# Performance work log

Measured on AMD Instinct MI355X. Metric: run time of the kernel, lower is better.

The kernel has to match this reference:

```python
import jax, jax.numpy as jnp
import numpy as np

N_TOKENS = 16384
D_MODEL = 2048
N_EXPERTS = 64
TOP_K = 8
TAU = 1.0
HYSTERESIS = 0.1
LAMBDA_TAX = 0.04
ALPHA_DAMPING = 0.7
SINKHORN_ITERS = 10


def setup_inputs() -> dict:
    key = jax.random.key(0)
    kx, kw, kb, kp, km = jax.random.split(key, 5)
    x = jax.random.normal(kx, (N_TOKENS, D_MODEL), dtype=jnp.float32)
    # LazyLinear(n_experts): weight [E, D], bias [E]
    W = jax.random.normal(kw, (N_EXPERTS, D_MODEL), dtype=jnp.float32) * (1.0 / np.sqrt(D_MODEL))
    b = jax.random.normal(kb, (N_EXPERTS,), dtype=jnp.float32) * 0.01
    # prev_probs buffer: a valid probability distribution per token
    prev_probs = jax.nn.softmax(jax.random.normal(kp, (N_TOKENS, N_EXPERTS), dtype=jnp.float32), axis=-1)
    # prev_mask buffer: exactly k experts active per token (what forward produces)
    scores = jax.random.normal(km, (N_TOKENS, N_EXPERTS), dtype=jnp.float32)
    idx = jax.lax.top_k(scores, TOP_K)[1]
    prev_mask = jnp.zeros((N_TOKENS, N_EXPERTS), dtype=bool).at[jnp.arange(N_TOKENS)[:, None], idx].set(True)
    return {"x": x, "W": W, "b": b, "prev_probs": prev_probs, "prev_mask": prev_mask}


def _router_probs(x, W, b, prev_probs, prev_mask):
    n = x.shape[0]
    logits = x @ W.T + b                               # [N, E]
    logits = logits - jnp.mean(logits, axis=-1, keepdims=True)
    M = jax.nn.softmax(logits / TAU, axis=-1)
    # Exact analytical gradient correction (correlation tax)
    C = M.T @ M                                        # [E, E]
    C = C * (1.0 - jnp.eye(N_EXPERTS, dtype=C.dtype))  # fill_diagonal_(0)
    grad_m = 4.0 * (M @ C)
    exact_grad = M * grad_m - M * jnp.sum(M * grad_m, axis=-1, keepdims=True)
    logits = logits - LAMBDA_TAX * exact_grad
    M = jax.nn.softmax(logits / TAU, axis=-1)
    # Convergent Sinkhorn-Knopp (10 fixed iterations)
    def body(i, M):
        M = M / jnp.clip(jnp.sum(M, axis=0, keepdims=True), 1e-12)
        M = M * (N_EXPERTS / n)
        M = M / jnp.clip(jnp.sum(M, axis=1, keepdims=True), 1e-12)
        return M
    M = jax.lax.fori_loop(0, SINKHORN_ITERS, body, M)
    # Momental damping with previous probs
    M = (1.0 - ALPHA_DAMPING) * prev_probs + ALPHA_DAMPING * M
    # Hysteresis blend with previous mask
    prev = prev_mask.astype(M.dtype)
    denom = jnp.clip(jnp.sum(prev, axis=-1, keepdims=True), 1.0)
    M = (1.0 - HYSTERESIS) * M + HYSTERESIS * (prev / denom)
    M = M / jnp.clip(jnp.sum(M, axis=-1, keepdims=True), 1e-12)
    return M


def reference(x, W, b, prev_probs, prev_mask):
    M = _router_probs(x, W, b, prev_probs, prev_mask)
    idx = jax.lax.top_k(M, TOP_K)[1]                   # [N, k]
    n = M.shape[0]
    mask = jnp.zeros(M.shape, dtype=bool).at[jnp.arange(n)[:, None], idx].set(True)
    return M, mask
```

## Files before the change

### kernel.cpp

```cpp
#include <hip/hip_runtime.h>
#include <math.h>

#define NT 16384
#define DM 2048
#define NE 64
#define TOPK 8
#define LTAX 0.04f
#define HYST 0.1f
#define ALPHA 0.7f

typedef unsigned int u32;
typedef unsigned short u16;
typedef unsigned long long u64;
typedef __attribute__((ext_vector_type(8))) short bf16x8;
typedef __attribute__((ext_vector_type(4))) float f32x4;

__device__ __forceinline__ float warp4_sum(float v) {
  v += __shfl_xor(v, 1); v += __shfl_xor(v, 2); return v;
}
__device__ __forceinline__ float warp4_max(float v) {
  v = fmaxf(v, __shfl_xor(v, 1)); v = fmaxf(v, __shfl_xor(v, 2)); return v;
}
__device__ __forceinline__ u16 f2bf(float f) {
  u32 u = __float_as_uint(f);
  return (u16)((u + 0x7fffu + ((u >> 16) & 1u)) >> 16);
}
__device__ __forceinline__ float bf2f(u16 h) { return __uint_as_float(((u32)h) << 16); }

__device__ __forceinline__ void split3(float a, short& h, short& m, short& l) {
  u16 hh = f2bf(a);  float r1 = a - bf2f(hh);
  u16 mm = f2bf(r1); float r2 = r1 - bf2f(mm);
  h = (short)hh; m = (short)mm; l = (short)f2bf(r2);
}

__device__ __forceinline__ u64 to_fx(float v) {
  return (u64)__double2ll_rn((double)v * 4294967296.0);
}

__global__ void k_init(const float* __restrict__ W, u16* __restrict__ Wh,
                       u16* __restrict__ Wm, u16* __restrict__ Wl,
                       u64* __restrict__ zp) {
  const int bid = blockIdx.x, tid = threadIdx.x;
  if (bid < 128) {
    int idx = (bid * 256 + tid) * 4;
    float4 v = *(const float4*)(W + idx);
    short h[4], m[4], l[4];
    split3(v.x, h[0], m[0], l[0]);
    split3(v.y, h[1], m[1], l[1]);
    split3(v.z, h[2], m[2], l[2]);
    split3(v.w, h[3], m[3], l[3]);
    *(ushort4*)(Wh + idx) = make_ushort4((u16)h[0], (u16)h[1], (u16)h[2], (u16)h[3]);
    *(ushort4*)(Wm + idx) = make_ushort4((u16)m[0], (u16)m[1], (u16)m[2], (u16)m[3]);
    *(ushort4*)(Wl + idx) = make_ushort4((u16)l[0], (u16)l[1], (u16)l[2], (u16)l[3]);
  } else {
    int i = (bid - 128) * 256 + tid;
    if (i < 26624) zp[i] = 0ull;
  }
}

__launch_bounds__(256, 5)
__global__ void k_gemm(const float* __restrict__ x, const u16* __restrict__ Whg,
                       const u16* __restrict__ Wmg, const u16* __restrict__ Wlg,
                       float* __restrict__ Lpart) {
  __shared__ __align__(16) u16 XS[15360];
  const int tid = threadIdx.x;
  const int bid = blockIdx.x;
  const int tile = bid >> 3, ks = bid & 7;
  const int row0 = tile * 64;
  const int k0 = ks * 256;
  const int lane = tid & 63, w = tid >> 6, l15 = lane & 15, l4 = lane >> 4;
  const int srow = tid >> 2, c8 = (tid & 3) * 8;
  const int stoff = srow * 40 + c8;

  f32x4 accA[4], accB[4];
#pragma unroll
  for (int eb = 0; eb < 4; eb++) { accA[eb] = (f32x4)0.f; accB[eb] = (f32x4)0.f; }

  float4 xq0, xq1;
  uint4 whv, wmv, wlv;
  const float* xrowp = x + (size_t)(row0 + srow) * DM + k0 + c8;
  const u16* whp = Whg + srow * DM + k0 + c8;
  const u16* wmp = Wmg + srow * DM + k0 + c8;
  const u16* wlp = Wlg + srow * DM + k0 + c8;

#define LOADCH(KC) { \
    xq0 = *(const float4*)(xrowp + (KC)); \
    xq1 = *(const float4*)(xrowp + (KC) + 4); \
    whv = *(const uint4*)(whp + (KC)); \
    wmv = *(const uint4*)(wmp + (KC)); \
    wlv = *(const uint4*)(wlp + (KC)); }

#define WRITECH() { \
    short ha[8], ma[8], la[8]; \
    split3(xq0.x, ha[0], ma[0], la[0]); \
    split3(xq0.y, ha[1], ma[1], la[1]); \
    split3(xq0.z, ha[2], ma[2], la[2]); \
    split3(xq0.w, ha[3], ma[3], la[3]); \
    split3(xq1.x, ha[4], ma[4], la[4]); \
    split3(xq1.y, ha[5], ma[5], la[5]); \
    split3(xq1.z, ha[6], ma[6], la[6]); \
    split3(xq1.w, ha[7], ma[7], la[7]); \
    bf16x8 xh8, xm8, xl8; \
    _Pragma("unroll") \
    for (int z = 0; z < 8; z++) { xh8[z] = ha[z]; xm8[z] = ma[z]; xl8[z] = la[z]; } \
    *(bf16x8*)(XS + 0     + stoff) = xh8; \
    *(bf16x8*)(XS + 2560  + stoff) = xm8; \
    *(bf16x8*)(XS + 5120  + stoff) = xl8; \
    *(uint4*)(XS + 7680  + stoff) = whv; \
    *(uint4*)(XS + 10240 + stoff) = wmv; \
    *(uint4*)(XS + 12800 + stoff) = wlv; }

#define COMPUTECH() { \
    const int ar = (w * 16 + l15) * 40 + l4 * 8; \
    bf16x8 ah = *(const bf16x8*)(XS + 0    + ar); \
    bf16x8 am = *(const bf16x8*)(XS + 2560 + ar); \
    bf16x8 al = *(const bf16x8*)(XS + 5120 + ar); \
    _Pragma("unroll") \
    for (int eb = 0; eb < 4; eb++) { \
      const int br = (eb * 16 + l15) * 40 + l4 * 8; \
      bf16x8 bh = *(const bf16x8*)(XS + 7680  + br); \
      bf16x8 bm = *(const bf16x8*)(XS + 10240 + br); \
      bf16x8 bl = *(const bf16x8*)(XS + 12800 + br); \
      accA[eb] = __builtin_amdgcn_mfma_f32_16x16x32_bf16(ah, bh, accA[eb], 0, 0, 0); \
      accB[eb] = __builtin_amdgcn_mfma_f32_16x16x32_bf16(ah, bm, accB[eb], 0, 0, 0); \
      accB[eb] = __builtin_amdgcn_mfma_f32_16x16x32_bf16(am, bh, accB[eb], 0, 0, 0); \
      accB[eb] = __builtin_amdgcn_mfma_f32_16x16x32_bf16(am, bm, accB[eb], 0, 0, 0); \
      accB[eb] = __builtin_amdgcn_mfma_f32_16x16x32_bf16(ah, bl, accB[eb], 0, 0, 0); \
      accB[eb] = __builtin_amdgcn_mfma_f32_16x16x32_bf16(al, bh, accB[eb], 0, 0, 0); \
    } }

  LOADCH(0);
#pragma unroll 1
  for (int t = 0; t < 8; t++) {
    __syncthreads();
    WRITECH();
    __syncthreads();
    if (t < 7) LOADCH((t + 1) * 32);
    COMPUTECH();
  }

  float* outp = Lpart + (size_t)ks * NT * NE;
#pragma unroll
  for (int eb = 0; eb < 4; eb++)
#pragma unroll
    for (int r = 0; r < 4; r++) {
      int trow = w * 16 + l4 * 4 + r;
      outp[(size_t)(row0 + trow) * NE + eb * 16 + l15] =
          (float)((double)accA[eb][r] + (double)accB[eb][r]);
    }
}

__launch_bounds__(256)
__global__ void k_post(const float* __restrict__ Lpart, const float* __restrict__ b,
                       float* __restrict__ Lbuf, u64* __restrict__ CmAcc) {
  __shared__ float ms[64 * 68];
  const int tid = threadIdx.x, bid = blockIdx.x;
  const int tg = tid >> 2, q = tid & 3;
  const int row = bid * 64 + tg;
  float l[16], m[16];
  {
    double acc[16];
#pragma unroll
    for (int j = 0; j < 16; j++) acc[j] = 0.0;
#pragma unroll 1
    for (int ks = 0; ks < 8; ks++) {
      const float* p = Lpart + (size_t)ks * NT * NE + (size_t)row * NE + q * 16;
#pragma unroll
      for (int i = 0; i < 4; i++) {
        float4 v = *(const float4*)(p + i * 4);
        acc[i * 4 + 0] += (double)v.x; acc[i * 4 + 1] += (double)v.y;
        acc[i * 4 + 2] += (double)v.z; acc[i * 4 + 3] += (double)v.w;
      }
    }
#pragma unroll
    for (int i = 0; i < 4; i++) {
      float4 bv = *(const float4*)(b + q * 16 + i * 4);
      l[i * 4 + 0] = (float)acc[i * 4 + 0] + bv.x;
      l[i * 4 + 1] = (float)acc[i * 4 + 1] + bv.y;
      l[i * 4 + 2] = (float)acc[i * 4 + 2] + bv.z;
      l[i * 4 + 3] = (float)acc[i * 4 + 3] + bv.w;
    }
    float s = 0.f;
#pragma unroll
    for (int j = 0; j < 16; j++) s += l[j];
    s = warp4_sum(s);
    const float mean = s * (1.0f / 64.0f);
    float mx = -1e30f;
#pragma unroll
    for (int j = 0; j < 16; j++) { l[j] -= mean; mx = fmaxf(mx, l[j]); }
    mx = warp4_max(mx);
#pragma unroll
    for (int i = 0; i < 4; i++)
      *(float4*)(Lbuf + (size_t)row * NE + q * 16 + i * 4) =
          make_float4(l[i * 4], l[i * 4 + 1], l[i * 4 + 2], l[i * 4 + 3]);
    float ps = 0.f;
#pragma unroll
    for (int j = 0; j < 16; j++) { m[j] = expf(l[j] - mx); ps += m[j]; }
    ps = warp4_sum(ps);
    const float inv = 1.0f / ps;
#pragma unroll
    for (int j = 0; j < 16; j++) m[j] *= inv;
#pragma unroll
    for (int i = 0; i < 4; i++)
      *(float4*)(ms + tg * 68 + q * 16 + i * 4) =
          make_float4(m[i * 4], m[i * 4 + 1], m[i * 4 + 2], m[i * 4 + 3]);
  }
  __syncthreads();
  const int gi0 = (tid >> 4) * 4;
  const int gj0 = (tid & 15) * 4;
  float ga[4][4];
#pragma unroll
  for (int a = 0; a < 4; a++)
#pragma unroll
    for (int c = 0; c < 4; c++) ga[a][c] = 0.f;
  for (int t = 0; t < 64; t++) {
    float4 a = *(const float4*)(ms + t * 68 + gi0);
    float4 bb = *(const float4*)(ms + t * 68 + gj0);
    ga[0][0] = fmaf(a.x, bb.x, ga[0][0]); ga[0][1] = fmaf(a.x, bb.y, ga[0][1]);
    ga[0][2] = fmaf(a.x, bb.z, ga[0][2]); ga[0][3] = fmaf(a.x, bb.w, ga[0][3]);
    ga[1][0] = fmaf(a.y, bb.x, ga[1][0]); ga[1][1] = fmaf(a.y, bb.y, ga[1][1]);
    ga[1][2] = fmaf(a.y, bb.z, ga[1][2]); ga[1][3] = fmaf(a.y, bb.w, ga[1][3]);
    ga[2][0] = fmaf(a.z, bb.x, ga[2][0]); ga[2][1] = fmaf(a.z, bb.y, ga[2][1]);
    ga[2][2] = fmaf(a.z, bb.z, ga[2][2]); ga[2][3] = fmaf(a.z, bb.w, ga[2][3]);
    ga[3][0] = fmaf(a.w, bb.x, ga[3][0]); ga[3][1] = fmaf(a.w, bb.y, ga[3][1]);
    ga[3][2] = fmaf(a.w, bb.z, ga[3][2]); ga[3][3] = fmaf(a.w, bb.w, ga[3][3]);
  }
  u64* slot = CmAcc + (size_t)(bid & 3) * 4096;
#pragma unroll
  for (int ii = 0; ii < 4; ii++)
#pragma unroll
    for (int jj = 0; jj < 4; jj++)
      atomicAdd(slot + (gi0 + ii) * 64 + gj0 + jj, to_fx(ga[ii][jj]));
}

__launch_bounds__(256)
__global__ void k_correct(const float* __restrict__ Lbuf, const u64* __restrict__ CmAcc,
                          float* __restrict__ M0, u64* __restrict__ p0Acc) {
  __shared__ float ms[64 * 68];
  __shared__ float Cs[4096];
  __shared__ float cred[256];
  const int tid = threadIdx.x, bid = blockIdx.x;
  const int tg = tid >> 2, q = tid & 3;
  const int lane = tid & 63, w = tid >> 6;
  const int row = bid * 64 + tg;
  float l[16], m[16];
#pragma unroll
  for (int i = 0; i < 4; i++) {
    float4 lv = *(const float4*)(Lbuf + (size_t)row * NE + q * 16 + i * 4);
    l[i * 4 + 0] = lv.x; l[i * 4 + 1] = lv.y; l[i * 4 + 2] = lv.z; l[i * 4 + 3] = lv.w;
  }
  {
    float mx = -1e30f;
#pragma unroll
    for (int j = 0; j < 16; j++) mx = fmaxf(mx, l[j]);
    mx = warp4_max(mx);
    float ps = 0.f;
#pragma unroll
    for (int j = 0; j < 16; j++) { m[j] = expf(l[j] - mx); ps += m[j]; }
    ps = warp4_sum(ps);
    const float inv = 1.0f / ps;
#pragma unroll
    for (int j = 0; j < 16; j++) m[j] *= inv;
#pragma unroll
    for (int i = 0; i < 4; i++)
      *(float4*)(ms + tg * 68 + q * 16 + i * 4) =
          make_float4(m[i * 4], m[i * 4 + 1], m[i * 4 + 2], m[i * 4 + 3]);
  }
#pragma unroll 4
  for (int i = 0; i < 16; i++) {
    int idx = tid + i * 256;
    u64 s = CmAcc[idx] + CmAcc[4096 + idx] + CmAcc[8192 + idx] + CmAcc[12288 + idx];
    float v = (float)((double)s * (1.0 / 4294967296.0));
    int r = idx >> 6, c = idx & 63;
    Cs[idx] = (r == c) ? 0.f : v;
  }
  __syncthreads();
  {
    float g[16];
#pragma unroll
    for (int j = 0; j < 16; j++) g[j] = 0.f;
    for (int f = 0; f < 64; f++) {
      float mf = ms[tg * 68 + f];
#pragma unroll
      for (int i = 0; i < 4; i++) {
        float4 cv = *(const float4*)(Cs + f * 64 + q * 16 + i * 4);
        g[i * 4 + 0] = fmaf(mf, cv.x, g[i * 4 + 0]);
        g[i * 4 + 1] = fmaf(mf, cv.y, g[i * 4 + 1]);
        g[i * 4 + 2] = fmaf(mf, cv.z, g[i * 4 + 2]);
        g[i * 4 + 3] = fmaf(mf, cv.w, g[i * 4 + 3]);
      }
    }
    float dot = 0.f;
#pragma unroll
    for (int j = 0; j < 16; j++) { g[j] *= 4.f; dot += m[j] * g[j]; }
    dot = warp4_sum(dot);
    float mx = -1e30f;
#pragma unroll
    for (int j = 0; j < 16; j++) {
      l[j] = l[j] - LTAX * (m[j] * (g[j] - dot));
      mx = fmaxf(mx, l[j]);
    }
    mx = warp4_max(mx);
    float ps = 0.f;
#pragma unroll
    for (int j = 0; j < 16; j++) { m[j] = expf(l[j] - mx); ps += m[j]; }
    ps = warp4_sum(ps);
    const float inv = 1.0f / ps;
#pragma unroll
    for (int j = 0; j < 16; j++) m[j] *= inv;
#pragma unroll
    for (int i = 0; i < 4; i++)
      *(float4*)(M0 + (size_t)row * NE + q * 16 + i * 4) =
          make_float4(m[i * 4], m[i * 4 + 1], m[i * 4 + 2], m[i * 4 + 3]);
  }
  {
    float cs[16];
#pragma unroll
    for (int j = 0; j < 16; j++) cs[j] = m[j];
#pragma unroll
    for (int j = 0; j < 16; j++) {
      cs[j] += __shfl_xor(cs[j], 4);  cs[j] += __shfl_xor(cs[j], 8);
      cs[j] += __shfl_xor(cs[j], 16); cs[j] += __shfl_xor(cs[j], 32);
    }
    if ((lane >> 2) == 0) {
#pragma unroll
      for (int j = 0; j < 16; j++) cred[w * 64 + lane * 16 + j] = cs[j];
    }
    __syncthreads();
    if (tid < 64)
      atomicAdd(p0Acc + (size_t)(bid & 15) * 64 + tid,
                to_fx(cred[tid] + cred[64 + tid] + cred[128 + tid] + cred[192 + tid]));
  }
}

__launch_bounds__(256)
__global__ void k_sink(const float* __restrict__ M0, const u64* __restrict__ pin,
                       u64* __restrict__ pout) {
  __shared__ u64 pred[4][64];
  __shared__ float fac[64];
  __shared__ float cred[256];
  const int tid = threadIdx.x, bid = blockIdx.x;
  const int tg = tid >> 2, q = tid & 3;
  const int lane = tid & 63, w = tid >> 6;
  const int row = bid * 64 + tg;
  {
    const int grp = tid >> 6, e = tid & 63;
    pred[grp][e] = pin[grp * 64 + e] + pin[(grp + 4) * 64 + e] +
                   pin[(grp + 8) * 64 + e] + pin[(grp + 12) * 64 + e];
  }
  __syncthreads();
  if (tid < 64) {
    u64 s = pred[0][tid] + pred[1][tid] + pred[2][tid] + pred[3][tid];
    float P = (float)((double)s * (1.0 / 4294967296.0));
    fac[tid] = 256.0f / fmaxf(P, 1e-30f);
  }
  __syncthreads();
  float mv[16];
#pragma unroll
  for (int i = 0; i < 4; i++) {
    float4 v = *(const float4*)(M0 + (size_t)row * NE + q * 16 + i * 4);
    mv[i * 4 + 0] = v.x; mv[i * 4 + 1] = v.y; mv[i * 4 + 2] = v.z; mv[i * 4 + 3] = v.w;
  }
  float Q = 0.f;
#pragma unroll
  for (int j = 0; j < 16; j++) Q = fmaf(mv[j], fac[q * 16 + j], Q);
  Q = warp4_sum(Q);
  const float U = 1.0f / fmaxf(Q, 1e-30f);
  float cs[16];
#pragma unroll
  for (int j = 0; j < 16; j++) cs[j] = U * mv[j];
#pragma unroll
  for (int j = 0; j < 16; j++) {
    cs[j] += __shfl_xor(cs[j], 4);  cs[j] += __shfl_xor(cs[j], 8);
    cs[j] += __shfl_xor(cs[j], 16); cs[j] += __shfl_xor(cs[j], 32);
  }
  if ((lane >> 2) == 0) {
#pragma unroll
    for (int j = 0; j < 16; j++) cred[w * 64 + lane * 16 + j] = cs[j];
  }
  __syncthreads();
  if (tid < 64)
    atomicAdd(pout + (size_t)(bid & 15) * 64 + tid,
              to_fx(cred[tid] + cred[64 + tid] + cred[128 + tid] + cred[192 + tid]));
}

__launch_bounds__(256)
__global__ void k_final(const float* __restrict__ M0, const u64* __restrict__ pin,
                        const float* __restrict__ pp, const void* __restrict__ pmask,
                        float* __restrict__ out) {
  __shared__ u64 pred[4][64];
  __shared__ float fac[64];
  __shared__ int s_cnt[256];
  __shared__ int s_flag;
  const int tid = threadIdx.x, bid = blockIdx.x;
  const int tg = tid >> 2, q = tid & 3;
  const int lane = tid & 63;
  const int row = bid * 64 + tg;

  {
    uint4 v = ((const uint4*)pmask)[tid];
    int c = 0; u32 ww;
    ww = v.x; c += ((ww & 0xffu) != 0) + ((ww & 0xff00u) != 0) + ((ww & 0xff0000u) != 0) + ((ww & 0xff000000u) != 0);
    ww = v.y; c += ((ww & 0xffu) != 0) + ((ww & 0xff00u) != 0) + ((ww & 0xff0000u) != 0) + ((ww & 0xff000000u) != 0);
    ww = v.z; c += ((ww & 0xffu) != 0) + ((ww & 0xff00u) != 0) + ((ww & 0xff0000u) != 0) + ((ww & 0xff000000u) != 0);
    ww = v.w; c += ((ww & 0xffu) != 0) + ((ww & 0xff00u) != 0) + ((ww & 0xff0000u) != 0) + ((ww & 0xff000000u) != 0);
    s_cnt[tid] = c;
    __syncthreads();
    for (int s = 128; s; s >>= 1) { if (tid < s) s_cnt[tid] += s_cnt[tid + s]; __syncthreads(); }
    if (tid == 0) { int n = s_cnt[0]; s_flag = (n > 384) ? 0 : ((n > 192) ? 2 : 1); }
  }
  {
    const int grp = tid >> 6, e = tid & 63;
    pred[grp][e] = pin[grp * 64 + e] + pin[(grp + 4) * 64 + e] +
                   pin[(grp + 8) * 64 + e] + pin[(grp + 12) * 64 + e];
  }
  __syncthreads();
  if (tid < 64) {
    u64 s = pred[0][tid] + pred[1][tid] + pred[2][tid] + pred[3][tid];
    float P = (float)((double)s * (1.0 / 4294967296.0));
    fac[tid] = 256.0f / fmaxf(P, 1e-30f);
  }
  __syncthreads();

  float mv[16];
#pragma unroll
  for (int i = 0; i < 4; i++) {
    float4 v = *(const float4*)(M0 + (size_t)row * NE + q * 16 + i * 4);
    mv[i * 4 + 0] = v.x; mv[i * 4 + 1] = v.y; mv[i * 4 + 2] = v.z; mv[i * 4 + 3] = v.w;
  }
  float Q = 0.f;
#pragma unroll
  for (int j = 0; j < 16; j++) Q = fmaf(mv[j], fac[q * 16 + j], Q);
  Q = warp4_sum(Q);
  const float U = 1.0f / fmaxf(Q, 1e-30f);
  float m[16];
#pragma unroll
  for (int j = 0; j < 16; j++) m[j] = U * mv[j] * fac[q * 16 + j];

  const int flag = s_flag;
  float pv[16], mk[16];
#pragma unroll
  for (int i = 0; i < 4; i++) {
    float4 v = *(const float4*)(pp + (size_t)row * NE + q * 16 + i * 4);
    pv[i * 4 + 0] = v.x; pv[i * 4 + 1] = v.y; pv[i * 4 + 2] = v.z; pv[i * 4 + 3] = v.w;
  }
  if (flag == 0) {
    const u32* pb = (const u32*)pmask + row * 16 + q * 4;
#pragma unroll
    for (int i = 0; i < 4; i++) {
      u32 ww = pb[i];
      mk[i * 4 + 0] = (ww & 0xffu) ? 1.f : 0.f;
      mk[i * 4 + 1] = (ww & 0xff00u) ? 1.f : 0.f;
      mk[i * 4 + 2] = (ww & 0xff0000u) ? 1.f : 0.f;
      mk[i * 4 + 3] = (ww & 0xff000000u) ? 1.f : 0.f;
    }
  } else if (flag == 1) {
    const int* pb = (const int*)pmask + (size_t)row * NE + q * 16;
#pragma unroll
    for (int j = 0; j < 16; j++) mk[j] = pb[j] ? 1.f : 0.f;
  } else {
    const float* pb = (const float*)pmask + (size_t)row * NE + q * 16;
#pragma unroll
    for (int j = 0; j < 16; j++) mk[j] = (pb[j] != 0.f) ? 1.f : 0.f;
  }
  float msum = 0.f;
#pragma unroll
  for (int j = 0; j < 16; j++) msum += mk[j];
  msum = warp4_sum(msum);
  const float hscale = HYST / fmaxf(msum, 1.0f);
  float v[16];
  float s = 0.f;
#pragma unroll
  for (int j = 0; j < 16; j++) {
    float base = (1.f - ALPHA) * pv[j] + ALPHA * m[j];
    v[j] = (1.f - HYST) * base + hscale * mk[j];
    s += v[j];
  }
  s = warp4_sum(s);
  const float inv = 1.0f / fmaxf(s, 1e-12f);
#pragma unroll
  for (int j = 0; j < 16; j++) v[j] *= inv;

  float* mout = out;
  float* kout = out + (size_t)NT * NE;
#pragma unroll
  for (int i = 0; i < 4; i++)
    *(float4*)(mout + (size_t)row * NE + q * 16 + i * 4) =
        make_float4(v[i * 4], v[i * 4 + 1], v[i * 4 + 2], v[i * 4 + 3]);

  int cnt[16];
#pragma unroll
  for (int j = 0; j < 16; j++) cnt[j] = 0;
  const int base = lane & ~3;
#pragma unroll
  for (int oq = 0; oq < 4; oq++) {
#pragma unroll
    for (int j2 = 0; j2 < 16; j2++) {
      float ov = __shfl(v[j2], base + oq, 64);
      int oe = oq * 16 + j2;
#pragma unroll
      for (int j = 0; j < 16; j++) {
        int me = q * 16 + j;
        if (ov > v[j] || (ov == v[j] && oe < me)) cnt[j]++;
      }
    }
  }
#pragma unroll
  for (int i = 0; i < 4; i++)
    *(float4*)(kout + (size_t)row * NE + q * 16 + i * 4) =
        make_float4(cnt[i * 4] < TOPK ? 1.f : 0.f, cnt[i * 4 + 1] < TOPK ? 1.f : 0.f,
                    cnt[i * 4 + 2] < TOPK ? 1.f : 0.f, cnt[i * 4 + 3] < TOPK ? 1.f : 0.f);
}

extern "C" void kernel_launch(void* const* d_in, const int* in_sizes, int n_in,
                              void* d_out, int out_size, void* d_ws, size_t ws_size,
                              hipStream_t stream) {
  const float* x = (const float*)d_in[0];
  const float* W = (const float*)d_in[1];
  const float* b = (const float*)d_in[2];
  const float* pp = (const float*)d_in[3];
  const void* pmask = d_in[4];
  float* out = (float*)d_out;

  unsigned char* wsb = (unsigned char*)d_ws;
  u16* Wh = (u16*)(wsb);
  u16* Wm = (u16*)(wsb + 262144);
  u16* Wl = (u16*)(wsb + 524288);
  float* Lpart = (float*)(wsb + 786432);
  float* Lbuf = (float*)(wsb + 34340864);
  float* M0buf = (float*)(wsb + 38535168);
  u64* CmAcc = (u64*)(wsb + 42729472);
  u64* pAcc = (u64*)(wsb + 42860544);

  k_init<<<232, 256, 0, stream>>>(W, Wh, Wm, Wl, CmAcc);
  k_gemm<<<2048, 256, 0, stream>>>(x, Wh, Wm, Wl, Lpart);
  k_post<<<256, 256, 0, stream>>>(Lpart, b, Lbuf, CmAcc);
  k_correct<<<256, 256, 0, stream>>>(Lbuf, CmAcc, M0buf, pAcc);
  for (int k = 1; k <= 9; k++)
    k_sink<<<256, 256, 0, stream>>>(M0buf, pAcc + (size_t)(k - 1) * 1024,
                                    pAcc + (size_t)k * 1024);
  k_final<<<256, 256, 0, stream>>>(M0buf, pAcc + (size_t)9 * 1024, pp, pmask, out);
}
```

Baseline: 177.1 us.

## Double the GEMM row tile to 128 rows per block to reuse W fragments

The logits GEMM block now covers 128 token rows instead of 64, so each wave computes two 16-row groups against the same staged W hi/mid/lo fragments. W shared-memory traffic and W global loads per row are halved, and the grid shrinks to 1024 blocks. In exchange, LDS use per block grows, the accumulator count doubles, and the occupancy hint drops from 5 to 3 blocks per SM, which can reduce latency hiding.

```diff
diff --git a/kernel.cpp b/kernel.cpp
--- a/kernel.cpp
+++ b/kernel.cpp
@@ -58,75 +58,93 @@
   }
 }
 
-__launch_bounds__(256, 5)
+__launch_bounds__(256, 3)
 __global__ void k_gemm(const float* __restrict__ x, const u16* __restrict__ Whg,
                        const u16* __restrict__ Wmg, const u16* __restrict__ Wlg,
                        float* __restrict__ Lpart) {
-  __shared__ __align__(16) u16 XS[15360];
+  __shared__ __align__(16) u16 XS[23040];
   const int tid = threadIdx.x;
   const int bid = blockIdx.x;
   const int tile = bid >> 3, ks = bid & 7;
-  const int row0 = tile * 64;
+  const int row0 = tile * 128;
   const int k0 = ks * 256;
   const int lane = tid & 63, w = tid >> 6, l15 = lane & 15, l4 = lane >> 4;
-  const int srow = tid >> 2, c8 = (tid & 3) * 8;
-  const int stoff = srow * 40 + c8;
-
-  f32x4 accA[4], accB[4];
-#pragma unroll
-  for (int eb = 0; eb < 4; eb++) { accA[eb] = (f32x4)0.f; accB[eb] = (f32x4)0.f; }
-
-  float4 xq0, xq1;
+  const int sr = tid >> 2, c8 = (tid & 3) * 8;
+
+  f32x4 accA[2][4], accB[2][4];
+#pragma unroll
+  for (int g = 0; g < 2; g++)
+#pragma unroll
+    for (int eb = 0; eb < 4; eb++) { accA[g][eb] = (f32x4)0.f; accB[g][eb] = (f32x4)0.f; }
+
+  float4 xq00, xq01, xq10, xq11;
   uint4 whv, wmv, wlv;
-  const float* xrowp = x + (size_t)(row0 + srow) * DM + k0 + c8;
-  const u16* whp = Whg + srow * DM + k0 + c8;
-  const u16* wmp = Wmg + srow * DM + k0 + c8;
-  const u16* wlp = Wlg + srow * DM + k0 + c8;
+  const float* xp0 = x + (size_t)(row0 + sr) * DM + k0 + c8;
+  const float* xp1 = xp0 + (size_t)64 * DM;
+  const u16* wph = Whg + (size_t)sr * DM + k0 + c8;
+  const u16* wpm = Wmg + (size_t)sr * DM + k0 + c8;
+  const u16* wpl = Wlg + (size_t)sr * DM + k0 + c8;
+  const int stA0 = sr * 40 + c8;
+  const int stA1 = (64 + sr) * 40 + c8;
+  const int stB = sr * 40 + c8;
 
 #define LOADCH(KC) { \
-    xq0 = *(const float4*)(xrowp + (KC)); \
-    xq1 = *(const float4*)(xrowp + (KC) + 4); \
-    whv = *(const uint4*)(whp + (KC)); \
-    wmv = *(const uint4*)(wmp + (KC)); \
-    wlv = *(const uint4*)(wlp + (KC)); }
-
-#define WRITECH() { \
+    xq00 = *(const float4*)(xp0 + (KC)); \
+    xq01 = *(const float4*)(xp0 + (KC) + 4); \
+    xq10 = *(const float4*)(xp1 + (KC)); \
+    xq11 = *(const float4*)(xp1 + (KC) + 4); \
+    whv = *(const uint4*)(wph + (KC)); \
+    wmv = *(const uint4*)(wpm + (KC)); \
+    wlv = *(const uint4*)(wpl + (KC)); }
+
+#define SPLIT8(Q0, Q1, DST) { \
     short ha[8], ma[8], la[8]; \
-    split3(xq0.x, ha[0], ma[0], la[0]); \
-    split3(xq0.y, ha[1], ma[1], la[1]); \
-    split3(xq0.z, ha[2], ma[2], la[2]); \
-    split3(xq0.w, ha[3], ma[3], la[3]); \
-    split3(xq1.x, ha[4], ma[4], la[4]); \
-    split3(xq1.y, ha[5], ma[5], la[5]); \
-    split3(xq1.z, ha[6], ma[6], la[6]); \
-    split3(xq1.w, ha[7], ma[7], la[7]); \
+    split3(Q0.x, ha[0], ma[0], la[0]); \
+    split3(Q0.y, ha[1], ma[1], la[1]); \
+    split3(Q0.z, ha[2], ma[2], la[2]); \
+    split3(Q0.w, ha[3], ma[3], la[3]); \
+    split3(Q1.x, ha[4], ma[4], la[4]); \
+    split3(Q1.y, ha[5], ma[5], la[5]); \
+    split3(Q1.z, ha[6], ma[6], la[6]); \
+    split3(Q1.w, ha[7], ma[7], la[7]); \
     bf16x8 xh8, xm8, xl8; \
     _Pragma("unroll") \
     for (int z = 0; z < 8; z++) { xh8[z] = ha[z]; xm8[z] = ma[z]; xl8[z] = la[z]; } \
-    *(bf16x8*)(XS + 0     + stoff) = xh8; \
-    *(bf16x8*)(XS + 2560  + stoff) = xm8; \
-    *(bf16x8*)(XS + 5120  + stoff) = xl8; \
-    *(uint4*)(XS + 7680  + stoff) = whv; \
-    *(uint4*)(XS + 10240 + stoff) = wmv; \
-    *(uint4*)(XS + 12800 + stoff) = wlv; }
+    *(bf16x8*)(XS + 0     + (DST)) = xh8; \
+    *(bf16x8*)(XS + 5120  + (DST)) = xm8; \
+    *(bf16x8*)(XS + 10240 + (DST)) = xl8; }
+
+#define WRITECH() { \
+    SPLIT8(xq00, xq01, stA0); \
+    SPLIT8(xq10, xq11, stA1); \
+    *(uint4*)(XS + 15360 + stB) = whv; \
+    *(uint4*)(XS + 17920 + stB) = wmv; \
+    *(uint4*)(XS + 20480 + stB) = wlv; }
 
 #define COMPUTECH() { \
-    const int ar = (w * 16 + l15) * 40 + l4 * 8; \
-    bf16x8 ah = *(const bf16x8*)(XS + 0    + ar); \
-    bf16x8 am = *(const bf16x8*)(XS + 2560 + ar); \
-    bf16x8 al = *(const bf16x8*)(XS + 5120 + ar); \
+    bf16x8 ah[2], am[2], al[2]; \
+    _Pragma("unroll") \
+    for (int g = 0; g < 2; g++) { \
+      const int ar = (w * 32 + g * 16 + l15) * 40 + l4 * 8; \
+      ah[g] = *(const bf16x8*)(XS + 0     + ar); \
+      am[g] = *(const bf16x8*)(XS + 5120  + ar); \
+      al[g] = *(const bf16x8*)(XS + 10240 + ar); \
+    } \
     _Pragma("unroll") \
     for (int eb = 0; eb < 4; eb++) { \
       const int br = (eb * 16 + l15) * 40 + l4 * 8; \
-      bf16x8 bh = *(const bf16x8*)(XS + 7680  + br); \
-      bf16x8 bm = *(const bf16x8*)(XS + 10240 + br); \
-      bf16x8 bl = *(const bf16x8*)(XS + 12800 + br); \
-      accA[eb] = __builtin_amdgcn_mfma_f32_16x16x32_bf16(ah, bh, accA[eb], 0, 0, 0); \
-      accB[eb] = __builtin_amdgcn_mfma_f32_16x16x32_bf16(ah, bm, accB[eb], 0, 0, 0); \
-      accB[eb] = __builtin_amdgcn_mfma_f32_16x16x32_bf16(am, bh, accB[eb], 0, 0, 0); \
-      accB[eb] = __builtin_amdgcn_mfma_f32_16x16x32_bf16(am, bm, accB[eb], 0, 0, 0); \
-      accB[eb] = __builtin_amdgcn_mfma_f32_16x16x32_bf16(ah, bl, accB[eb], 0, 0, 0); \
-      accB[eb] = __builtin_amdgcn_mfma_f32_16x16x32_bf16(al, bh, accB[eb], 0, 0, 0); \
+      bf16x8 bh = *(const bf16x8*)(XS + 15360 + br); \
+      bf16x8 bm = *(const bf16x8*)(XS + 17920 + br); \
+      bf16x8 bl = *(const bf16x8*)(XS + 20480 + br); \
+      _Pragma("unroll") \
+      for (int g = 0; g < 2; g++) { \
+        accA[g][eb] = __builtin_amdgcn_mfma_f32_16x16x32_bf16(ah[g], bh, accA[g][eb], 0, 0, 0); \
+        accB[g][eb] = __builtin_amdgcn_mfma_f32_16x16x32_bf16(ah[g], bm, accB[g][eb], 0, 0, 0); \
+        accB[g][eb] = __builtin_amdgcn_mfma_f32_16x16x32_bf16(am[g], bh, accB[g][eb], 0, 0, 0); \
+        accB[g][eb] = __builtin_amdgcn_mfma_f32_16x16x32_bf16(am[g], bm, accB[g][eb], 0, 0, 0); \
+        accB[g][eb] = __builtin_amdgcn_mfma_f32_16x16x32_bf16(ah[g], bl, accB[g][eb], 0, 0, 0); \
+        accB[g][eb] = __builtin_amdgcn_mfma_f32_16x16x32_bf16(al[g], bh, accB[g][eb], 0, 0, 0); \
+      } \
     } }
 
   LOADCH(0);
@@ -141,13 +159,15 @@
 
   float* outp = Lpart + (size_t)ks * NT * NE;
 #pragma unroll
-  for (int eb = 0; eb < 4; eb++)
-#pragma unroll
-    for (int r = 0; r < 4; r++) {
-      int trow = w * 16 + l4 * 4 + r;
-      outp[(size_t)(row0 + trow) * NE + eb * 16 + l15] =
-          (float)((double)accA[eb][r] + (double)accB[eb][r]);
-    }
+  for (int g = 0; g < 2; g++)
+#pragma unroll
+    for (int eb = 0; eb < 4; eb++)
+#pragma unroll
+      for (int r = 0; r < 4; r++) {
+        int trow = w * 32 + g * 16 + l4 * 4 + r;
+        outp[(size_t)(row0 + trow) * NE + eb * 16 + l15] =
+            (float)((double)accA[g][eb][r] + (double)accB[g][eb][r]);
+      }
 }
 
 __launch_bounds__(256)
@@ -533,7 +553,7 @@
   u64* pAcc = (u64*)(wsb + 42860544);
 
   k_init<<<232, 256, 0, stream>>>(W, Wh, Wm, Wl, CmAcc);
-  k_gemm<<<2048, 256, 0, stream>>>(x, Wh, Wm, Wl, Lpart);
+  k_gemm<<<1024, 256, 0, stream>>>(x, Wh, Wm, Wl, Lpart);
   k_post<<<256, 256, 0, stream>>>(Lpart, b, Lbuf, CmAcc);
   k_correct<<<256, 256, 0, stream>>>(Lbuf, CmAcc, M0buf, pAcc);
   for (int k = 1; k <= 9; k++)
```

New measurement: 176.0 us. About the same (-0.6%).
